# Optimization experiments

Measured on AMD Instinct MI355X. Metric: run time of the kernel, lower is better.

## Reference

```python
import jax, jax.numpy as jnp
import numpy as np

B = 256        # graph pairs
MAX_SET = 64   # nodes per graph == max_set_size (padding is identity)
E = 512        # edges per graph
D = 128        # node_state_dim == av.filters_3
T = 64         # av.transform_dim
N_PROP = 5
N_TIME = 3
TEMP = 0.1
SINK_ITERS = 20
NG = 2 * B
N = NG * MAX_SET
TOT_E = NG * E


def sinkhorn(log_alpha):
    la = log_alpha / TEMP
    for _ in range(SINK_ITERS):
        la = la - jax.nn.logsumexp(la, axis=2, keepdims=True)
        la = la - jax.nn.logsumexp(la, axis=1, keepdims=True)
    return jnp.exp(la)


def setup_inputs() -> dict:
    key = jax.random.key(0)
    ks = jax.random.split(key, 32)

    def lin(k, i, o):
        return jax.random.normal(k, (i, o), jnp.float32) / np.sqrt(i).astype(np.float32)

    node_features = jax.random.normal(ks[0], (N, 32), jnp.float32)
    edge_features = jax.random.normal(ks[1], (TOT_E, 16), jnp.float32)
    offs = jnp.repeat(jnp.arange(NG, dtype=jnp.int32) * MAX_SET, E)
    from_idx = jax.random.randint(ks[2], (TOT_E,), 0, MAX_SET, jnp.int32) + offs
    to_idx = jax.random.randint(ks[3], (TOT_E,), 0, MAX_SET, jnp.int32) + offs
    return {
        "node_features": node_features, "edge_features": edge_features,
        "from_idx": from_idx, "to_idx": to_idx,
        "node_enc_w": lin(ks[4], 32, D), "node_enc_b": jnp.zeros((D,), jnp.float32),
        "edge_enc_w": lin(ks[5], 16, 64), "edge_enc_b": jnp.zeros((64,), jnp.float32),
        "mw1": lin(ks[6], 2 * D + 64, 2 * D), "mb1": jnp.zeros((2 * D,), jnp.float32),
        "mw2": lin(ks[7], 2 * D, D), "mb2": jnp.zeros((D,), jnp.float32),
        "nw1": lin(ks[8], 2 * D, 2 * D), "nb1": jnp.zeros((2 * D,), jnp.float32),
        "nw2": lin(ks[9], 2 * D, D), "nb2": jnp.zeros((D,), jnp.float32),
        "cw1": lin(ks[10], 2 * D, 2 * D), "cb1": jnp.zeros((2 * D,), jnp.float32),
        "cw2": lin(ks[11], 2 * D, D), "cb2": jnp.zeros((D,), jnp.float32),
        "t1w": lin(ks[12], D, T), "t1b": jnp.zeros((T,), jnp.float32),
        "t2w": lin(ks[13], T, T), "t2b": jnp.zeros((T,), jnp.float32),
    }


def reference(node_features, edge_features, from_idx, to_idx,
              node_enc_w, node_enc_b, edge_enc_w, edge_enc_b,
              mw1, mb1, mw2, mb2, nw1, nb1, nw2, nb2,
              cw1, cb1, cw2, cb2, t1w, t1b, t2w, t2b):
    # Encoder (GMN GraphEncoder: linear maps on raw node/edge features)
    h0 = node_features @ node_enc_w + node_enc_b          # [N, D]
    e0 = edge_features @ edge_enc_w + edge_enc_b          # [TOT_E, 64]
    store = jnp.zeros((N, D * (N_PROP + 1)), h0.dtype)    # node_feature_store
    plan = None
    for _t in range(N_TIME):
        h = h0
        parts = [jnp.zeros((N, D), h0.dtype)]             # slot 0 stays zero
        for p in range(1, N_PROP + 1):
            inter = store[:, (p - 1) * D: p * D]          # time_update_idx == 'k_t'
            comb = jax.nn.relu(jnp.concatenate([h, inter], 1) @ cw1 + cb1) @ cw2 + cb2
            # GraphPropLayer: gather -> message MLP -> segment_sum -> node update MLP
            msg_in = jnp.concatenate([comb[from_idx], comb[to_idx], e0], 1)
            messages = jax.nn.relu(msg_in @ mw1 + mb1) @ mw2 + mb2
            agg = jax.ops.segment_sum(messages, to_idx, num_segments=N)
            h = jax.nn.relu(jnp.concatenate([comb, agg], 1) @ nw1 + nb1) @ nw2 + nb2
            parts.append(h)
        store = jnp.concatenate(parts, 1)                 # [N, D*(K+1)]
        # split into padded query/corpus stacks (all graphs have MAX_SET nodes,
        # so F.pad and the size masks are identity here)
        s = store.reshape(NG, MAX_SET, -1)
        q, c = s[0::2], s[1::2]                           # [B, M, D*(K+1)]
        tq = jax.nn.relu(q[:, :, -D:] @ t1w + t1b) @ t2w + t2b
        tc = jax.nn.relu(c[:, :, -D:] @ t1w + t1b) @ t2w + t2b
        sim = jnp.einsum('bqt,bct->bqc', tq, tc)
        plan = sinkhorn(sim)                              # node transport plan [B,M,M]
        qfc = jnp.einsum('bqc,bcd->bqd', plan, c)
        cfq = jnp.einsum('bqc,bqd->bcd', plan, q)
        inter_feats = jnp.stack([qfc, cfq], 1)[:, :, :, D:].reshape(N, N_PROP * D)
        store = store.at[:, D:].set(inter_feats)
    return plan
```

## Files before the change

### kernel.cpp

```cpp
#include <hip/hip_runtime.h>
#include <hip/hip_bf16.h>

#define NNODES   32768
#define NGROUPS  512
#define EPG      512
#define ND       (32768l*128)

typedef __attribute__((ext_vector_type(4))) float f32x4;
typedef __attribute__((ext_vector_type(8))) short bf16x8;

__device__ __forceinline__ short f2bf(float x) {
  unsigned u = __float_as_uint(x);
  unsigned r = (u + 0x7FFF + ((u >> 16) & 1)) >> 16;
  return (short)r;
}
__device__ __forceinline__ float bf2f(short h) {
  return __uint_as_float(((unsigned)(unsigned short)h) << 16);
}
__device__ __forceinline__ void split3(float x, short* ph, short* pm, short* pl, long idx) {
  short h = f2bf(x); float r1 = x - bf2f(h);
  short m = f2bf(r1); float r2 = r1 - bf2f(m);
  ph[idx] = h; pm[idx] = m; pl[idx] = f2bf(r2);
}

__global__ void k_node_enc(const float* __restrict__ nf, const float* __restrict__ w,
                           const float* __restrict__ b, float* __restrict__ h0) {
  int idx = blockIdx.x * 256 + threadIdx.x;
  int row = idx >> 7, col = idx & 127;
  const float* x = nf + row * 32;
  float acc = b[col];
#pragma unroll
  for (int k = 0; k < 32; ++k) acc = fmaf(x[k], w[k * 128 + col], acc);
  h0[idx] = acc;
}

__global__ void k_prep(const float* __restrict__ eew, const float* __restrict__ eeb,
                       const float* __restrict__ mw1, const float* __restrict__ mb1,
                       const float* __restrict__ mb2, const float* __restrict__ nw1,
                       float* __restrict__ Wfold, float* __restrict__ bfold,
                       float* __restrict__ vbias) {
  const int c = threadIdx.x, b = blockIdx.x;
  if (b < 16) {
    float a = 0.f;
    for (int j = 0; j < 64; ++j) a = fmaf(eew[b * 64 + j], mw1[(256 + j) * 256 + c], a);
    Wfold[b * 256 + c] = a;
  } else if (b == 16) {
    float a = mb1[c];
    for (int j = 0; j < 64; ++j) a = fmaf(eeb[j], mw1[(256 + j) * 256 + c], a);
    bfold[c] = a;
  } else {
    float a = 0.f;
    for (int j = 0; j < 128; ++j) a = fmaf(mb2[j], nw1[(128 + j) * 256 + c], a);
    vbias[c] = a;
  }
}

__global__ void k_wsplit3(const float* __restrict__ W, int C, int Kd,
                          short* __restrict__ th, short* __restrict__ tm,
                          short* __restrict__ tl) {
  const int c = blockIdx.x;
  for (int k = threadIdx.x; k < Kd; k += 256) {
    float w = W[(long)k * C + c];
    split3(w, th, tm, tl, c * 256 + k);
  }
}

__global__ void k_csr(const int* __restrict__ from_idx, const int* __restrict__ to_idx,
                      const float* __restrict__ ef,
                      int* __restrict__ csr_f, int* __restrict__ rp_g,
                      float* __restrict__ efp, int* __restrict__ deg) {
  __shared__ int cnt[64], rps[65];
  __shared__ int tls[EPG], fls[EPG];
  __shared__ short ord[EPG];
  const int g = blockIdx.x, tid = threadIdx.x;
  const int be = g * EPG, bn = g * 64;
  if (tid < 64) cnt[tid] = 0;
  __syncthreads();
  for (int e = tid; e < EPG; e += 256) {
    int t = to_idx[be + e] - bn;
    tls[e] = t;
    fls[e] = from_idx[be + e] - bn;
    atomicAdd(&cnt[t], 1);
  }
  __syncthreads();
  if (tid == 0) {
    int s = 0;
    for (int i = 0; i < 64; ++i) { rps[i] = s; s += cnt[i]; }
    rps[64] = s;
  }
  __syncthreads();
  if (tid < 64) {
    int pos = rps[tid];
    for (int e = 0; e < EPG; ++e)
      if (tls[e] == tid) ord[pos++] = (short)e;
  }
  __syncthreads();
  for (int ec = tid; ec < EPG; ec += 256) {
    const int eo = ord[ec];
    csr_f[be + ec] = fls[eo];
    const float4* src = (const float4*)&ef[(long)(be + eo) * 16];
    float4* dst = (float4*)&efp[(long)(be + ec) * 16];
    dst[0] = src[0]; dst[1] = src[1]; dst[2] = src[2]; dst[3] = src[3];
  }
  if (tid < 65) rp_g[g * 65 + tid] = rps[tid];
  if (tid < 64) deg[bn + tid] = cnt[tid];
}

template<int KTOT, bool DEG, bool SUM2, bool RPX0, bool WPOUT>
__global__ __launch_bounds__(256, 3)
void k_mlp2m(const float* __restrict__ x0,
             const short* __restrict__ x0h, const short* __restrict__ x0m,
             const short* __restrict__ x0l,
             const float* __restrict__ x1, const float* __restrict__ x1b,
             const short* __restrict__ W1h, const short* __restrict__ W1m,
             const short* __restrict__ W1l,
             const float* __restrict__ b1, const int* __restrict__ deg,
             const float* __restrict__ vbias,
             const short* __restrict__ W2h, const short* __restrict__ W2m,
             const short* __restrict__ W2l,
             const float* __restrict__ b2,
             float* __restrict__ out,
             short* __restrict__ outh, short* __restrict__ outm,
             short* __restrict__ outl) {
  __shared__ short xh[32 * 264];
  __shared__ short xm[32 * 264];
  __shared__ short xl[32 * 264];
  __shared__ int degs[32];
  const int tid = threadIdx.x;
  const long row0 = (long)blockIdx.x * 32;

  if constexpr (RPX0) {
    for (int i = tid; i < 32 * 16; i += 256) {
      const int r = i >> 4, q = i & 15;
      const long gb = (row0 + r) * 128 + q * 8;
      const int lb = r * 264 + q * 8;
      *(bf16x8*)&xh[lb] = *(const bf16x8*)&x0h[gb];
      *(bf16x8*)&xm[lb] = *(const bf16x8*)&x0m[gb];
      *(bf16x8*)&xl[lb] = *(const bf16x8*)&x0l[gb];
    }
  } else {
    for (int i = tid; i < 32 * 32; i += 256) {
      const int r = i >> 5, q = i & 31;
      float4 v = *(const float4*)&x0[(row0 + r) * 128 + q * 4];
      const int base = r * 264 + q * 4;
      split3(v.x, xh, xm, xl, base + 0);
      split3(v.y, xh, xm, xl, base + 1);
      split3(v.z, xh, xm, xl, base + 2);
      split3(v.w, xh, xm, xl, base + 3);
    }
  }
  if constexpr (KTOT == 256) {
    for (int i = tid; i < 32 * 32; i += 256) {
      const int r = i >> 5, q = i & 31;
      float4 v = *(const float4*)&x1[(row0 + r) * 128 + q * 4];
      if constexpr (SUM2) {
        float4 w = *(const float4*)&x1b[(row0 + r) * 128 + q * 4];
        v.x += w.x; v.y += w.y; v.z += w.z; v.w += w.w;
      }
      const int base = r * 264 + 128 + q * 4;
      split3(v.x, xh, xm, xl, base + 0);
      split3(v.y, xh, xm, xl, base + 1);
      split3(v.z, xh, xm, xl, base + 2);
      split3(v.w, xh, xm, xl, base + 3);
    }
  }
  if constexpr (DEG) { if (tid < 32) degs[tid] = deg[row0 + tid]; }
  __syncthreads();

  const int lane = tid & 63, wid = tid >> 6;
  const int lr = lane & 15;
  const int lk = (lane >> 4) * 8;
  const int rsub = (lane >> 4) * 4;

  f32x4 acc[2][4];
#pragma unroll
  for (int fc = 0; fc < 4; ++fc) {
    const int col = wid * 64 + fc * 16 + lr;
    const float bv = b1[col];
#pragma unroll
    for (int fr = 0; fr < 2; ++fr) acc[fr][fc] = {bv, bv, bv, bv};
    if constexpr (DEG) {
      const float vb = vbias[col];
#pragma unroll
      for (int fr = 0; fr < 2; ++fr)
#pragma unroll
        for (int r = 0; r < 4; ++r)
          acc[fr][fc][r] += (float)degs[fr * 16 + rsub + r] * vb;
    }
  }

#pragma unroll 2
  for (int ks = 0; ks < KTOT / 32; ++ks) {
    const int k0 = ks * 32 + lk;
    bf16x8 ah[2], am[2], al[2];
#pragma unroll
    for (int fr = 0; fr < 2; ++fr) {
      const int ab = (fr * 16 + lr) * 264 + k0;
      ah[fr] = *(const bf16x8*)&xh[ab];
      am[fr] = *(const bf16x8*)&xm[ab];
      al[fr] = *(const bf16x8*)&xl[ab];
    }
#pragma unroll
    for (int fc = 0; fc < 4; ++fc) {
      const long wrow = (long)(wid * 64 + fc * 16 + lr) * 256 + k0;
      const bf16x8 bh = *(const bf16x8*)&W1h[wrow];
      const bf16x8 bm = *(const bf16x8*)&W1m[wrow];
      const bf16x8 bl = *(const bf16x8*)&W1l[wrow];
#pragma unroll
      for (int fr = 0; fr < 2; ++fr) {
        acc[fr][fc] = __builtin_amdgcn_mfma_f32_16x16x32_bf16(ah[fr], bh, acc[fr][fc], 0, 0, 0);
        acc[fr][fc] = __builtin_amdgcn_mfma_f32_16x16x32_bf16(ah[fr], bm, acc[fr][fc], 0, 0, 0);
        acc[fr][fc] = __builtin_amdgcn_mfma_f32_16x16x32_bf16(am[fr], bh, acc[fr][fc], 0, 0, 0);
        acc[fr][fc] = __builtin_amdgcn_mfma_f32_16x16x32_bf16(ah[fr], bl, acc[fr][fc], 0, 0, 0);
        acc[fr][fc] = __builtin_amdgcn_mfma_f32_16x16x32_bf16(am[fr], bm, acc[fr][fc], 0, 0, 0);
        acc[fr][fc] = __builtin_amdgcn_mfma_f32_16x16x32_bf16(al[fr], bh, acc[fr][fc], 0, 0, 0);
      }
    }
  }
  __syncthreads();

#pragma unroll
  for (int fr = 0; fr < 2; ++fr)
#pragma unroll
    for (int fc = 0; fc < 4; ++fc) {
      const int col = wid * 64 + fc * 16 + lr;
#pragma unroll
      for (int r = 0; r < 4; ++r) {
        const int row = fr * 16 + rsub + r;
        float v = fmaxf(acc[fr][fc][r], 0.f);
        split3(v, xh, xm, xl, row * 264 + col);
      }
    }
  __syncthreads();

  f32x4 acc2[2][2];
#pragma unroll
  for (int fc = 0; fc < 2; ++fc) {
    const float bv = b2[wid * 32 + fc * 16 + lr];
#pragma unroll
    for (int fr = 0; fr < 2; ++fr) acc2[fr][fc] = {bv, bv, bv, bv};
  }
#pragma unroll 2
  for (int ks = 0; ks < 8; ++ks) {
    const int k0 = ks * 32 + lk;
    bf16x8 ah[2], am[2], al[2];
#pragma unroll
    for (int fr = 0; fr < 2; ++fr) {
      const int ab = (fr * 16 + lr) * 264 + k0;
      ah[fr] = *(const bf16x8*)&xh[ab];
      am[fr] = *(const bf16x8*)&xm[ab];
      al[fr] = *(const bf16x8*)&xl[ab];
    }
#pragma unroll
    for (int fc = 0; fc < 2; ++fc) {
      const long wrow = (long)(wid * 32 + fc * 16 + lr) * 256 + k0;
      const bf16x8 bh = *(const bf16x8*)&W2h[wrow];
      const bf16x8 bm = *(const bf16x8*)&W2m[wrow];
      const bf16x8 bl = *(const bf16x8*)&W2l[wrow];
#pragma unroll
      for (int fr = 0; fr < 2; ++fr) {
        acc2[fr][fc] = __builtin_amdgcn_mfma_f32_16x16x32_bf16(ah[fr], bh, acc2[fr][fc], 0, 0, 0);
        acc2[fr][fc] = __builtin_amdgcn_mfma_f32_16x16x32_bf16(ah[fr], bm, acc2[fr][fc], 0, 0, 0);
        acc2[fr][fc] = __builtin_amdgcn_mfma_f32_16x16x32_bf16(am[fr], bh, acc2[fr][fc], 0, 0, 0);
        acc2[fr][fc] = __builtin_amdgcn_mfma_f32_16x16x32_bf16(ah[fr], bl, acc2[fr][fc], 0, 0, 0);
        acc2[fr][fc] = __builtin_amdgcn_mfma_f32_16x16x32_bf16(am[fr], bm, acc2[fr][fc], 0, 0, 0);
        acc2[fr][fc] = __builtin_amdgcn_mfma_f32_16x16x32_bf16(al[fr], bh, acc2[fr][fc], 0, 0, 0);
      }
    }
  }
#pragma unroll
  for (int fr = 0; fr < 2; ++fr)
#pragma unroll
    for (int fc = 0; fc < 2; ++fc) {
      const int col = wid * 32 + fc * 16 + lr;
#pragma unroll
      for (int r = 0; r < 4; ++r) {
        const long gi = (row0 + fr * 16 + rsub + r) * 128 + col;
        if constexpr (WPOUT) {
          split3(acc2[fr][fc][r], outh, outm, outl, gi);
        } else {
          out[gi] = acc2[fr][fc][r];
        }
      }
    }
}

__global__ __launch_bounds__(256, 3)
void k_edgem(const short* __restrict__ chp, const short* __restrict__ cmp,
             const short* __restrict__ clp,
             const float* __restrict__ efp,
             const short* __restrict__ m1h, const short* __restrict__ m1m,
             const short* __restrict__ m1l,
             const short* __restrict__ m2h, const short* __restrict__ m2m,
             const short* __restrict__ m2l,
             const float* __restrict__ Wfold, const float* __restrict__ bfold,
             const int* __restrict__ csr_f, const int* __restrict__ rp_g,
             float* __restrict__ aggM) {
  __shared__ __align__(16) float cAB[2 * 64 * 68];
  __shared__ __align__(16) float ag[64 * 64];
  __shared__ short fl[EPG];
  __shared__ int rp[65];
  float* cA = cAB;
  float* cB = cAB + 64 * 68;
  short* agp = (short*)cAB;

  const int tid = threadIdx.x;
  const int g = blockIdx.x, half = blockIdx.y;
  const int be = g * EPG, bn = g * 64;

  for (int i = tid; i < EPG; i += 256) fl[i] = (short)csr_f[be + i];
  if (tid < 65) rp[tid] = rp_g[g * 65 + tid];

  const int lane = tid & 63, wid = tid >> 6;
  const int lr = lane & 15;
  const int lk = (lane >> 4) * 8;
  const int rsub = (lane >> 4) * 4;
  const int ng = tid >> 4, cg = tid & 15;
  const int n0 = ng * 4, cq = cg * 4;

  float* aggMh = aggM + (long)half * ND;

  for (int cbi = 0; cbi < 2; ++cbi) {
    const int col0 = (half * 2 + cbi) * 64;
    __syncthreads();

    {
      const int isB = wid >> 1;
      const int cw = (wid & 1) * 32;
      const int wkof = isB * 128;
      float* dstC = isB ? cB : cA;
#pragma unroll 1
      for (int hf = 0; hf < 2; ++hf) {
        f32x4 c[2][2];
#pragma unroll
        for (int fr = 0; fr < 2; ++fr)
#pragma unroll
          for (int fc = 0; fc < 2; ++fc) c[fr][fc] = {0.f, 0.f, 0.f, 0.f};
        for (int ks = 0; ks < 4; ++ks) {
          const int k0 = ks * 32 + lk;
          bf16x8 ah[2], am[2], al[2];
#pragma unroll
          for (int fr = 0; fr < 2; ++fr) {
            const long ga = (long)(bn + (hf * 2 + fr) * 16 + lr) * 128 + k0;
            ah[fr] = *(const bf16x8*)&chp[ga];
            am[fr] = *(const bf16x8*)&cmp[ga];
            al[fr] = *(const bf16x8*)&clp[ga];
          }
#pragma unroll
          for (int fc = 0; fc < 2; ++fc) {
            const long wrow = (long)(col0 + cw + fc * 16 + lr) * 256 + wkof + k0;
            const bf16x8 bh = *(const bf16x8*)&m1h[wrow];
            const bf16x8 bm = *(const bf16x8*)&m1m[wrow];
            const bf16x8 bl = *(const bf16x8*)&m1l[wrow];
#pragma unroll
            for (int fr = 0; fr < 2; ++fr) {
              c[fr][fc] = __builtin_amdgcn_mfma_f32_16x16x32_bf16(ah[fr], bh, c[fr][fc], 0, 0, 0);
              c[fr][fc] = __builtin_amdgcn_mfma_f32_16x16x32_bf16(ah[fr], bm, c[fr][fc], 0, 0, 0);
              c[fr][fc] = __builtin_amdgcn_mfma_f32_16x16x32_bf16(am[fr], bh, c[fr][fc], 0, 0, 0);
              c[fr][fc] = __builtin_amdgcn_mfma_f32_16x16x32_bf16(ah[fr], bl, c[fr][fc], 0, 0, 0);
              c[fr][fc] = __builtin_amdgcn_mfma_f32_16x16x32_bf16(am[fr], bm, c[fr][fc], 0, 0, 0);
              c[fr][fc] = __builtin_amdgcn_mfma_f32_16x16x32_bf16(al[fr], bh, c[fr][fc], 0, 0, 0);
            }
          }
        }
#pragma unroll
        for (int fr = 0; fr < 2; ++fr)
#pragma unroll
          for (int fc = 0; fc < 2; ++fc) {
            const int col = cw + fc * 16 + lr;
#pragma unroll
            for (int r = 0; r < 4; ++r)
              dstC[((hf * 2 + fr) * 16 + rsub + r) * 68 + col] = c[fr][fc][r];
          }
      }
    }
    float4 Wf[16];
#pragma unroll
    for (int k = 0; k < 16; ++k) Wf[k] = *(const float4*)&Wfold[k * 256 + col0 + cq];
    const float4 bf = *(const float4*)&bfold[col0 + cq];
    __syncthreads();

#pragma unroll
    for (int i = 0; i < 4; ++i) {
      const int n = n0 + i;
      const float4 cBn = *(const float4*)&cB[n * 68 + cq];
      const int eBeg = rp[n], eEnd = rp[n + 1];
      float4 acc0 = make_float4(0.f, 0.f, 0.f, 0.f);
      float4 acc1 = make_float4(0.f, 0.f, 0.f, 0.f);
      int e = eBeg;
      for (; e + 1 < eEnd; e += 2) {
        const int f0 = fl[e], f1 = fl[e + 1];
        const float* er0 = efp + (long)(be + e) * 16;
        const float* er1 = efp + (long)(be + e + 1) * 16;
        float4 ea[4], eb[4];
#pragma unroll
        for (int kq = 0; kq < 4; ++kq) { ea[kq] = ((const float4*)er0)[kq]; eb[kq] = ((const float4*)er1)[kq]; }
        float4 h0 = bf, h1 = bf;
#pragma unroll
        for (int kq = 0; kq < 4; ++kq) {
          const float ev0[4] = {ea[kq].x, ea[kq].y, ea[kq].z, ea[kq].w};
          const float ev1[4] = {eb[kq].x, eb[kq].y, eb[kq].z, eb[kq].w};
#pragma unroll
          for (int s = 0; s < 4; ++s) {
            const float4 w = Wf[kq * 4 + s];
            h0.x = fmaf(ev0[s], w.x, h0.x); h0.y = fmaf(ev0[s], w.y, h0.y);
            h0.z = fmaf(ev0[s], w.z, h0.z); h0.w = fmaf(ev0[s], w.w, h0.w);
            h1.x = fmaf(ev1[s], w.x, h1.x); h1.y = fmaf(ev1[s], w.y, h1.y);
            h1.z = fmaf(ev1[s], w.z, h1.z); h1.w = fmaf(ev1[s], w.w, h1.w);
          }
        }
        const float4 va0 = *(const float4*)&cA[f0 * 68 + cq];
        const float4 va1 = *(const float4*)&cA[f1 * 68 + cq];
        acc0.x += fmaxf(h0.x + va0.x + cBn.x, 0.f);
        acc0.y += fmaxf(h0.y + va0.y + cBn.y, 0.f);
        acc0.z += fmaxf(h0.z + va0.z + cBn.z, 0.f);
        acc0.w += fmaxf(h0.w + va0.w + cBn.w, 0.f);
        acc1.x += fmaxf(h1.x + va1.x + cBn.x, 0.f);
        acc1.y += fmaxf(h1.y + va1.y + cBn.y, 0.f);
        acc1.z += fmaxf(h1.z + va1.z + cBn.z, 0.f);
        acc1.w += fmaxf(h1.w + va1.w + cBn.w, 0.f);
      }
      if (e < eEnd) {
        const int f = fl[e];
        const float* er = efp + (long)(be + e) * 16;
        float4 h = bf;
#pragma unroll
        for (int kq = 0; kq < 4; ++kq) {
          const float4 e4 = ((const float4*)er)[kq];
          const float ev[4] = {e4.x, e4.y, e4.z, e4.w};
#pragma unroll
          for (int s = 0; s < 4; ++s) {
            const float4 w = Wf[kq * 4 + s];
            h.x = fmaf(ev[s], w.x, h.x); h.y = fmaf(ev[s], w.y, h.y);
            h.z = fmaf(ev[s], w.z, h.z); h.w = fmaf(ev[s], w.w, h.w);
          }
        }
        const float4 va = *(const float4*)&cA[f * 68 + cq];
        acc0.x += fmaxf(h.x + va.x + cBn.x, 0.f);
        acc0.y += fmaxf(h.y + va.y + cBn.y, 0.f);
        acc0.z += fmaxf(h.z + va.z + cBn.z, 0.f);
        acc0.w += fmaxf(h.w + va.w + cBn.w, 0.f);
      }
      acc0.x += acc1.x; acc0.y += acc1.y; acc0.z += acc1.z; acc0.w += acc1.w;
      *(float4*)&ag[n * 64 + cq] = acc0;
    }
    __syncthreads();

    for (int i = tid; i < 1024; i += 256) {
      const int n = i >> 4, kq = (i & 15) * 4;
      const float4 v = *(const float4*)&ag[n * 64 + kq];
      const int b0 = n * 72 + kq;
      split3(v.x, agp, agp + 4608, agp + 9216, b0 + 0);
      split3(v.y, agp, agp + 4608, agp + 9216, b0 + 1);
      split3(v.z, agp, agp + 4608, agp + 9216, b0 + 2);
      split3(v.w, agp, agp + 4608, agp + 9216, b0 + 3);
    }
    __syncthreads();

    {
      f32x4 aM2[4][2];
#pragma unroll
      for (int fr = 0; fr < 4; ++fr)
#pragma unroll
        for (int fc = 0; fc < 2; ++fc) aM2[fr][fc] = {0.f, 0.f, 0.f, 0.f};

      for (int ks = 0; ks < 2; ++ks) {
        const int k0 = ks * 32 + lk;
        bf16x8 ah[4], am[4], al[4];
#pragma unroll
        for (int fr = 0; fr < 4; ++fr) {
          const int ab = (fr * 16 + lr) * 72 + k0;
          ah[fr] = *(const bf16x8*)&agp[ab];
          am[fr] = *(const bf16x8*)&agp[4608 + ab];
          al[fr] = *(const bf16x8*)&agp[9216 + ab];
        }
#pragma unroll
        for (int fc = 0; fc < 2; ++fc) {
          const long wrow = (long)(wid * 32 + fc * 16 + lr) * 256 + col0 + k0;
          const bf16x8 bh = *(const bf16x8*)&m2h[wrow];
          const bf16x8 bm = *(const bf16x8*)&m2m[wrow];
          const bf16x8 bl = *(const bf16x8*)&m2l[wrow];
#pragma unroll
          for (int fr = 0; fr < 4; ++fr) {
            aM2[fr][fc] = __builtin_amdgcn_mfma_f32_16x16x32_bf16(ah[fr], bh, aM2[fr][fc], 0, 0, 0);
            aM2[fr][fc] = __builtin_amdgcn_mfma_f32_16x16x32_bf16(ah[fr], bm, aM2[fr][fc], 0, 0, 0);
            aM2[fr][fc] = __builtin_amdgcn_mfma_f32_16x16x32_bf16(am[fr], bh, aM2[fr][fc], 0, 0, 0);
            aM2[fr][fc] = __builtin_amdgcn_mfma_f32_16x16x32_bf16(ah[fr], bl, aM2[fr][fc], 0, 0, 0);
            aM2[fr][fc] = __builtin_amdgcn_mfma_f32_16x16x32_bf16(am[fr], bm, aM2[fr][fc], 0, 0, 0);
            aM2[fr][fc] = __builtin_amdgcn_mfma_f32_16x16x32_bf16(al[fr], bh, aM2[fr][fc], 0, 0, 0);
          }
        }
      }
      if (cbi == 0) {
#pragma unroll
        for (int fr = 0; fr < 4; ++fr)
#pragma unroll
          for (int fc = 0; fc < 2; ++fc) {
            const int col = wid * 32 + fc * 16 + lr;
#pragma unroll
            for (int r = 0; r < 4; ++r)
              aggMh[(long)(bn + fr * 16 + rsub + r) * 128 + col] = aM2[fr][fc][r];
          }
      } else {
#pragma unroll
        for (int fr = 0; fr < 4; ++fr)
#pragma unroll
          for (int fc = 0; fc < 2; ++fc) {
            const int col = wid * 32 + fc * 16 + lr;
#pragma unroll
            for (int r = 0; r < 4; ++r)
              atomicAdd(&aggMh[(long)(bn + fr * 16 + rsub + r) * 128 + col], aM2[fr][fc][r]);
          }
      }
    }
  }
}

__global__ void k_tfeat(const float* __restrict__ x,
                        const float* __restrict__ t1w, const float* __restrict__ t1b,
                        const float* __restrict__ t2w, const float* __restrict__ t2b,
                        float* __restrict__ tf) {
  __shared__ float xs[4][128];
  __shared__ float ys[4][64];
  const int tid = threadIdx.x;
  const long row0 = (long)blockIdx.x * 4;
  for (int i = tid; i < 512; i += 256)
    xs[i >> 7][i & 127] = x[(row0 + (i >> 7)) * 128 + (i & 127)];
  __syncthreads();
  const int r = tid >> 6, c = tid & 63;
  float acc = t1b[c];
#pragma unroll 4
  for (int k = 0; k < 128; ++k) acc = fmaf(xs[r][k], t1w[k * 64 + c], acc);
  ys[r][c] = fmaxf(acc, 0.f);
  __syncthreads();
  float a2 = t2b[c];
#pragma unroll 4
  for (int k = 0; k < 64; ++k) a2 = fmaf(ys[r][k], t2w[k * 64 + c], a2);
  tf[(row0 + r) * 64 + c] = a2;
}

__global__ void k_sim(const float* __restrict__ tf, float* __restrict__ sim) {
  const int b = blockIdx.x, tid = threadIdx.x;
  __shared__ float tq[64][65];
  __shared__ float tcs[64][65];
  for (int i = tid; i < 4096; i += 256) {
    tq[i >> 6][i & 63]  = tf[(long)b * 8192 + i];
    tcs[i >> 6][i & 63] = tf[(long)b * 8192 + 4096 + i];
  }
  __syncthreads();
  const int m = tid >> 2, j0 = (tid & 3) * 16;
#pragma unroll
  for (int j = 0; j < 16; ++j) {
    float a = 0.f;
#pragma unroll 4
    for (int k = 0; k < 64; ++k) a = fmaf(tq[m][k], tcs[j0 + j][k], a);
    sim[(long)b * 4096 + m * 64 + j0 + j] = a;
  }
}

__global__ void k_sink(float* __restrict__ sim, float* __restrict__ outp) {
  const int b = blockIdx.x, tid = threadIdx.x;
  __shared__ float la[64][65];
  const float C = 14.426950408889634f;
  for (int i = tid; i < 4096; i += 256)
    la[i >> 6][i & 63] = sim[(long)b * 4096 + i] * C;
  __syncthreads();
  const int r4 = tid >> 2, l4 = tid & 3;
  for (int it = 0; it < 20; ++it) {
    {
      float m = -3.4e38f;
#pragma unroll
      for (int i = 0; i < 16; ++i) m = fmaxf(m, la[r4][l4 + 4 * i]);
      m = fmaxf(m, __shfl_xor(m, 1)); m = fmaxf(m, __shfl_xor(m, 2));
      float s = 0.f;
#pragma unroll
      for (int i = 0; i < 16; ++i) s += exp2f(la[r4][l4 + 4 * i] - m);
      s += __shfl_xor(s, 1); s += __shfl_xor(s, 2);
      const float lse = m + log2f(s);
#pragma unroll
      for (int i = 0; i < 16; ++i) la[r4][l4 + 4 * i] -= lse;
    }
    __syncthreads();
    {
      float m = -3.4e38f;
#pragma unroll
      for (int i = 0; i < 16; ++i) m = fmaxf(m, la[l4 + 4 * i][r4]);
      m = fmaxf(m, __shfl_xor(m, 1)); m = fmaxf(m, __shfl_xor(m, 2));
      float s = 0.f;
#pragma unroll
      for (int i = 0; i < 16; ++i) s += exp2f(la[l4 + 4 * i][r4] - m);
      s += __shfl_xor(s, 1); s += __shfl_xor(s, 2);
      const float lse = m + log2f(s);
#pragma unroll
      for (int i = 0; i < 16; ++i) la[l4 + 4 * i][r4] -= lse;
    }
    __syncthreads();
  }
  for (int i = tid; i < 4096; i += 256) {
    const float v = exp2f(la[i >> 6][i & 63]);
    outp[(long)b * 4096 + i] = v;
    sim[(long)b * 4096 + i] = v;
  }
}

__global__ void k_mix(const float* __restrict__ plan, const float* __restrict__ src,
                      float* __restrict__ dst) {
  const int b = blockIdx.x, tid = threadIdx.x;
  __shared__ float pl[64][65];
  __shared__ float qs[64][128];
  __shared__ float cs[64][128];
  const long qbase = (long)(2 * b) * 64, cbase = qbase + 64;
  for (int i = tid; i < 4096; i += 256) pl[i >> 6][i & 63] = plan[(long)b * 4096 + i];
  for (int i = tid; i < 8192; i += 256) {
    qs[i >> 7][i & 127] = src[qbase * 128 + i];
    cs[i >> 7][i & 127] = src[cbase * 128 + i];
  }
  __syncthreads();
  const int d = tid & 127, m0 = (tid >> 7) * 32;
  for (int m = m0; m < m0 + 32; ++m) {
    float a = 0.f;
#pragma unroll 4
    for (int j = 0; j < 64; ++j) a = fmaf(pl[m][j], cs[j][d], a);
    dst[(qbase + m) * 128 + d] = a;
  }
  for (int j = m0; j < m0 + 32; ++j) {
    float a = 0.f;
#pragma unroll 4
    for (int m = 0; m < 64; ++m) a = fmaf(pl[m][j], qs[m][d], a);
    dst[(cbase + j) * 128 + d] = a;
  }
}

extern "C" void kernel_launch(void* const* d_in, const int* in_sizes, int n_in,
                              void* d_out, int out_size, void* d_ws, size_t ws_size,
                              hipStream_t stream) {
  const float* nf  = (const float*)d_in[0];
  const float* ef  = (const float*)d_in[1];
  const int* from_idx = (const int*)d_in[2];
  const int* to_idx   = (const int*)d_in[3];
  const float* new_w = (const float*)d_in[4];
  const float* new_b = (const float*)d_in[5];
  const float* eew = (const float*)d_in[6];
  const float* eeb = (const float*)d_in[7];
  const float* mw1 = (const float*)d_in[8];
  const float* mb1 = (const float*)d_in[9];
  const float* mw2 = (const float*)d_in[10];
  const float* mb2 = (const float*)d_in[11];
  const float* nw1 = (const float*)d_in[12];
  const float* nb1 = (const float*)d_in[13];
  const float* nw2 = (const float*)d_in[14];
  const float* nb2 = (const float*)d_in[15];
  const float* cw1 = (const float*)d_in[16];
  const float* cb1 = (const float*)d_in[17];
  const float* cw2 = (const float*)d_in[18];
  const float* cb2 = (const float*)d_in[19];
  const float* t1w = (const float*)d_in[20];
  const float* t1b = (const float*)d_in[21];
  const float* t2w = (const float*)d_in[22];
  const float* t2b = (const float*)d_in[23];

  float* W = (float*)d_ws;
  float* h0     = W;
  float* aggM0  = h0 + ND;
  float* aggM1  = aggM0 + ND;
  float* parts  = aggM1 + ND;
  float* efp    = parts + 5 * ND;
  float* Wfold  = efp + 262144l * 16;
  float* bfold  = Wfold + 4096;
  float* vbias  = bfold + 256;
  int*   deg    = (int*)(vbias + 256);
  int*   csr_f  = deg + 32768;
  int*   rp_g   = csr_f + 262144;
  short* cw1t_h = (short*)(rp_g + 33280);
  short* cw1t_m = cw1t_h + 65536;
  short* cw1t_l = cw1t_m + 65536;
  short* nw1t_h = cw1t_l + 65536;
  short* nw1t_m = nw1t_h + 65536;
  short* nw1t_l = nw1t_m + 65536;
  short* cw2t_h = nw1t_l + 65536;
  short* cw2t_m = cw2t_h + 32768;
  short* cw2t_l = cw2t_m + 32768;
  short* nw2t_h = cw2t_l + 32768;
  short* nw2t_m = nw2t_h + 32768;
  short* nw2t_l = nw2t_m + 32768;
  short* m1t_h  = nw2t_l + 32768;
  short* m1t_m  = m1t_h + 65536;
  short* m1t_l  = m1t_m + 65536;
  short* m2t_h  = m1t_l + 65536;
  short* m2t_m  = m2t_h + 32768;
  short* m2t_l  = m2t_m + 32768;
  short* chp    = m2t_l + 32768;
  short* cmp    = chp + 32768l * 128;
  short* clp    = cmp + 32768l * 128;
  float* tf     = aggM0;
  float* sim    = aggM0 + 2097152;
  float* outp   = (float*)d_out;

  k_prep<<<18, 256, 0, stream>>>(eew, eeb, mw1, mb1, mb2, nw1, Wfold, bfold, vbias);
  k_csr<<<512, 256, 0, stream>>>(from_idx, to_idx, ef, csr_f, rp_g, efp, deg);
  k_wsplit3<<<256, 256, 0, stream>>>(cw1, 256, 256, cw1t_h, cw1t_m, cw1t_l);
  k_wsplit3<<<256, 256, 0, stream>>>(nw1, 256, 256, nw1t_h, nw1t_m, nw1t_l);
  k_wsplit3<<<128, 256, 0, stream>>>(cw2, 128, 256, cw2t_h, cw2t_m, cw2t_l);
  k_wsplit3<<<128, 256, 0, stream>>>(nw2, 128, 256, nw2t_h, nw2t_m, nw2t_l);
  k_wsplit3<<<256, 256, 0, stream>>>(mw1, 256, 256, m1t_h, m1t_m, m1t_l);
  k_wsplit3<<<128, 256, 0, stream>>>(mw2, 128, 256, m2t_h, m2t_m, m2t_l);
  k_node_enc<<<16384, 256, 0, stream>>>(nf, new_w, new_b, h0);

  for (int t = 0; t < 3; ++t) {
    const float* hprev = h0;
    for (int p = 1; p <= 5; ++p) {
      if (t > 0 && p > 1)
        k_mlp2m<256, false, false, false, true><<<1024, 256, 0, stream>>>(
            hprev, nullptr, nullptr, nullptr,
            parts + (long)(p - 1) * ND, nullptr,
            cw1t_h, cw1t_m, cw1t_l, cb1, nullptr, nullptr,
            cw2t_h, cw2t_m, cw2t_l, cb2, nullptr, chp, cmp, clp);
      else
        k_mlp2m<128, false, false, false, true><<<1024, 256, 0, stream>>>(
            hprev, nullptr, nullptr, nullptr, nullptr, nullptr,
            cw1t_h, cw1t_m, cw1t_l, cb1, nullptr, nullptr,
            cw2t_h, cw2t_m, cw2t_l, cb2, nullptr, chp, cmp, clp);
      k_edgem<<<dim3(512, 2), 256, 0, stream>>>(chp, cmp, clp, efp,
                                                m1t_h, m1t_m, m1t_l,
                                                m2t_h, m2t_m, m2t_l,
                                                Wfold, bfold, csr_f, rp_g, aggM0);
      float* hnew = parts + (long)(p - 1) * ND;
      k_mlp2m<256, true, true, true, false><<<1024, 256, 0, stream>>>(
          nullptr, chp, cmp, clp, aggM0, aggM1,
          nw1t_h, nw1t_m, nw1t_l, nb1, deg, vbias,
          nw2t_h, nw2t_m, nw2t_l, nb2, hnew, nullptr, nullptr, nullptr);
      hprev = hnew;
    }
    k_tfeat<<<8192, 256, 0, stream>>>(parts + 4 * ND, t1w, t1b, t2w, t2b, tf);
    k_sim<<<256, 256, 0, stream>>>(tf, sim);
    k_sink<<<256, 256, 0, stream>>>(sim, outp);
    if (t < 2) {
      for (int pi = 3; pi >= 0; --pi)
        k_mix<<<256, 256, 0, stream>>>(sim, parts + (long)pi * ND, parts + (long)(pi + 1) * ND);
    }
  }
}
```

Baseline: 6.118 ms.

## Split edge kernel into hidden-aggregation and separate mw2 GEMM kernels

The fused edge kernel used to compute the 256-wide hidden aggregate in two column halves, each applying mw2 and combining partial results through atomics and a second buffer. It is now split in two. An edge kernel over 4 column blocks writes the full aggregated hidden tensor to global memory, and a separate dense GEMM kernel applies mw2 with K=256, so the atomics and the SUM2 addition in the node MLP go away. This adds a global round trip of a 2*ND float buffer and one extra launch per propagation step, in exchange for more parallelism and simpler GEMM tiling.

```diff
diff --git a/kernel.cpp b/kernel.cpp
--- a/kernel.cpp
+++ b/kernel.cpp
@@ -106,12 +106,12 @@
   if (tid < 64) deg[bn + tid] = cnt[tid];
 }
 
-template<int KTOT, bool DEG, bool SUM2, bool RPX0, bool WPOUT>
+template<int KTOT, bool DEG, bool RPX0, bool WPOUT>
 __global__ __launch_bounds__(256, 3)
 void k_mlp2m(const float* __restrict__ x0,
              const short* __restrict__ x0h, const short* __restrict__ x0m,
              const short* __restrict__ x0l,
-             const float* __restrict__ x1, const float* __restrict__ x1b,
+             const float* __restrict__ x1,
              const short* __restrict__ W1h, const short* __restrict__ W1m,
              const short* __restrict__ W1l,
              const float* __restrict__ b1, const int* __restrict__ deg,
@@ -153,10 +153,6 @@
     for (int i = tid; i < 32 * 32; i += 256) {
       const int r = i >> 5, q = i & 31;
       float4 v = *(const float4*)&x1[(row0 + r) * 128 + q * 4];
-      if constexpr (SUM2) {
-        float4 w = *(const float4*)&x1b[(row0 + r) * 128 + q * 4];
-        v.x += w.x; v.y += w.y; v.z += w.z; v.w += w.w;
-      }
       const int base = r * 264 + 128 + q * 4;
       split3(v.x, xh, xm, xl, base + 0);
       split3(v.y, xh, xm, xl, base + 1);
@@ -286,27 +282,24 @@
 }
 
 __global__ __launch_bounds__(256, 3)
-void k_edgem(const short* __restrict__ chp, const short* __restrict__ cmp,
+void k_edgeb(const short* __restrict__ chp, const short* __restrict__ cmp,
              const short* __restrict__ clp,
              const float* __restrict__ efp,
              const short* __restrict__ m1h, const short* __restrict__ m1m,
              const short* __restrict__ m1l,
-             const short* __restrict__ m2h, const short* __restrict__ m2m,
-             const short* __restrict__ m2l,
              const float* __restrict__ Wfold, const float* __restrict__ bfold,
              const int* __restrict__ csr_f, const int* __restrict__ rp_g,
-             float* __restrict__ aggM) {
+             float* __restrict__ ag) {
   __shared__ __align__(16) float cAB[2 * 64 * 68];
-  __shared__ __align__(16) float ag[64 * 64];
   __shared__ short fl[EPG];
   __shared__ int rp[65];
   float* cA = cAB;
   float* cB = cAB + 64 * 68;
-  short* agp = (short*)cAB;
 
   const int tid = threadIdx.x;
-  const int g = blockIdx.x, half = blockIdx.y;
+  const int g = blockIdx.x, cb = blockIdx.y;
   const int be = g * EPG, bn = g * 64;
+  const int col0 = cb * 64;
 
   for (int i = tid; i < EPG; i += 256) fl[i] = (short)csr_f[be + i];
   if (tid < 65) rp[tid] = rp_g[g * 65 + tid];
@@ -318,202 +311,225 @@
   const int ng = tid >> 4, cg = tid & 15;
   const int n0 = ng * 4, cq = cg * 4;
 
-  float* aggMh = aggM + (long)half * ND;
-
-  for (int cbi = 0; cbi < 2; ++cbi) {
-    const int col0 = (half * 2 + cbi) * 64;
-    __syncthreads();
-
-    {
-      const int isB = wid >> 1;
-      const int cw = (wid & 1) * 32;
-      const int wkof = isB * 128;
-      float* dstC = isB ? cB : cA;
+  {
+    const int isB = wid >> 1;
+    const int cw = (wid & 1) * 32;
+    const int wkof = isB * 128;
+    float* dstC = isB ? cB : cA;
 #pragma unroll 1
-      for (int hf = 0; hf < 2; ++hf) {
-        f32x4 c[2][2];
-#pragma unroll
-        for (int fr = 0; fr < 2; ++fr)
-#pragma unroll
-          for (int fc = 0; fc < 2; ++fc) c[fr][fc] = {0.f, 0.f, 0.f, 0.f};
-        for (int ks = 0; ks < 4; ++ks) {
-          const int k0 = ks * 32 + lk;
-          bf16x8 ah[2], am[2], al[2];
+    for (int hf = 0; hf < 2; ++hf) {
+      f32x4 c[2][2];
+#pragma unroll
+      for (int fr = 0; fr < 2; ++fr)
+#pragma unroll
+        for (int fc = 0; fc < 2; ++fc) c[fr][fc] = {0.f, 0.f, 0.f, 0.f};
+      for (int ks = 0; ks < 4; ++ks) {
+        const int k0 = ks * 32 + lk;
+        bf16x8 ah[2], am[2], al[2];
+#pragma unroll
+        for (int fr = 0; fr < 2; ++fr) {
+          const long ga = (long)(bn + (hf * 2 + fr) * 16 + lr) * 128 + k0;
+          ah[fr] = *(const bf16x8*)&chp[ga];
+          am[fr] = *(const bf16x8*)&cmp[ga];
+          al[fr] = *(const bf16x8*)&clp[ga];
+        }
+#pragma unroll
+        for (int fc = 0; fc < 2; ++fc) {
+          const long wrow = (long)(col0 + cw + fc * 16 + lr) * 256 + wkof + k0;
+          const bf16x8 bh = *(const bf16x8*)&m1h[wrow];
+          const bf16x8 bm = *(const bf16x8*)&m1m[wrow];
+          const bf16x8 bl = *(const bf16x8*)&m1l[wrow];
 #pragma unroll
           for (int fr = 0; fr < 2; ++fr) {
-            const long ga = (long)(bn + (hf * 2 + fr) * 16 + lr) * 128 + k0;
-            ah[fr] = *(const bf16x8*)&chp[ga];
-            am[fr] = *(const bf16x8*)&cmp[ga];
-            al[fr] = *(const bf16x8*)&clp[ga];
-          }
-#pragma unroll
-          for (int fc = 0; fc < 2; ++fc) {
-            const long wrow = (long)(col0 + cw + fc * 16 + lr) * 256 + wkof + k0;
-            const bf16x8 bh = *(const bf16x8*)&m1h[wrow];
-            const bf16x8 bm = *(const bf16x8*)&m1m[wrow];
-            const bf16x8 bl = *(const bf16x8*)&m1l[wrow];
-#pragma unroll
-            for (int fr = 0; fr < 2; ++fr) {
-              c[fr][fc] = __builtin_amdgcn_mfma_f32_16x16x32_bf16(ah[fr], bh, c[fr][fc], 0, 0, 0);
-              c[fr][fc] = __builtin_amdgcn_mfma_f32_16x16x32_bf16(ah[fr], bm, c[fr][fc], 0, 0, 0);
-              c[fr][fc] = __builtin_amdgcn_mfma_f32_16x16x32_bf16(am[fr], bh, c[fr][fc], 0, 0, 0);
-              c[fr][fc] = __builtin_amdgcn_mfma_f32_16x16x32_bf16(ah[fr], bl, c[fr][fc], 0, 0, 0);
-              c[fr][fc] = __builtin_amdgcn_mfma_f32_16x16x32_bf16(am[fr], bm, c[fr][fc], 0, 0, 0);
-              c[fr][fc] = __builtin_amdgcn_mfma_f32_16x16x32_bf16(al[fr], bh, c[fr][fc], 0, 0, 0);
-            }
+            c[fr][fc] = __builtin_amdgcn_mfma_f32_16x16x32_bf16(ah[fr], bh, c[fr][fc], 0, 0, 0);
+            c[fr][fc] = __builtin_amdgcn_mfma_f32_16x16x32_bf16(ah[fr], bm, c[fr][fc], 0, 0, 0);
+            c[fr][fc] = __builtin_amdgcn_mfma_f32_16x16x32_bf16(am[fr], bh, c[fr][fc], 0, 0, 0);
+            c[fr][fc] = __builtin_amdgcn_mfma_f32_16x16x32_bf16(ah[fr], bl, c[fr][fc], 0, 0, 0);
+            c[fr][fc] = __builtin_amdgcn_mfma_f32_16x16x32_bf16(am[fr], bm, c[fr][fc], 0, 0, 0);
+            c[fr][fc] = __builtin_amdgcn_mfma_f32_16x16x32_bf16(al[fr], bh, c[fr][fc], 0, 0, 0);
           }
         }
-#pragma unroll
-        for (int fr = 0; fr < 2; ++fr)
-#pragma unroll
-          for (int fc = 0; fc < 2; ++fc) {
-            const int col = cw + fc * 16 + lr;
-#pragma unroll
-            for (int r = 0; r < 4; ++r)
-              dstC[((hf * 2 + fr) * 16 + rsub + r) * 68 + col] = c[fr][fc][r];
-          }
-      }
-    }
-    float4 Wf[16];
-#pragma unroll
-    for (int k = 0; k < 16; ++k) Wf[k] = *(const float4*)&Wfold[k * 256 + col0 + cq];
-    const float4 bf = *(const float4*)&bfold[col0 + cq];
-    __syncthreads();
-
-#pragma unroll
-    for (int i = 0; i < 4; ++i) {
-      const int n = n0 + i;
-      const float4 cBn = *(const float4*)&cB[n * 68 + cq];
-      const int eBeg = rp[n], eEnd = rp[n + 1];
-      float4 acc0 = make_float4(0.f, 0.f, 0.f, 0.f);
-      float4 acc1 = make_float4(0.f, 0.f, 0.f, 0.f);
-      int e = eBeg;
-      for (; e + 1 < eEnd; e += 2) {
-        const int f0 = fl[e], f1 = fl[e + 1];
-        const float* er0 = efp + (long)(be + e) * 16;
-        const float* er1 = efp + (long)(be + e + 1) * 16;
-        float4 ea[4], eb[4];
-#pragma unroll
-        for (int kq = 0; kq < 4; ++kq) { ea[kq] = ((const float4*)er0)[kq]; eb[kq] = ((const float4*)er1)[kq]; }
-        float4 h0 = bf, h1 = bf;
-#pragma unroll
-        for (int kq = 0; kq < 4; ++kq) {
-          const float ev0[4] = {ea[kq].x, ea[kq].y, ea[kq].z, ea[kq].w};
-          const float ev1[4] = {eb[kq].x, eb[kq].y, eb[kq].z, eb[kq].w};
-#pragma unroll
-          for (int s = 0; s < 4; ++s) {
-            const float4 w = Wf[kq * 4 + s];
-            h0.x = fmaf(ev0[s], w.x, h0.x); h0.y = fmaf(ev0[s], w.y, h0.y);
-            h0.z = fmaf(ev0[s], w.z, h0.z); h0.w = fmaf(ev0[s], w.w, h0.w);
-            h1.x = fmaf(ev1[s], w.x, h1.x); h1.y = fmaf(ev1[s], w.y, h1.y);
-            h1.z = fmaf(ev1[s], w.z, h1.z); h1.w = fmaf(ev1[s], w.w, h1.w);
-          }
+      }
+#pragma unroll
+      for (int fr = 0; fr < 2; ++fr)
+#pragma unroll
+        for (int fc = 0; fc < 2; ++fc) {
+          const int col = cw + fc * 16 + lr;
+#pragma unroll
+          for (int r = 0; r < 4; ++r)
+            dstC[((hf * 2 + fr) * 16 + rsub + r) * 68 + col] = c[fr][fc][r];
         }
-        const float4 va0 = *(const float4*)&cA[f0 * 68 + cq];
-        const float4 va1 = *(const float4*)&cA[f1 * 68 + cq];
-        acc0.x += fmaxf(h0.x + va0.x + cBn.x, 0.f);
-        acc0.y += fmaxf(h0.y + va0.y + cBn.y, 0.f);
-        acc0.z += fmaxf(h0.z + va0.z + cBn.z, 0.f);
-        acc0.w += fmaxf(h0.w + va0.w + cBn.w, 0.f);
-        acc1.x += fmaxf(h1.x + va1.x + cBn.x, 0.f);
-        acc1.y += fmaxf(h1.y + va1.y + cBn.y, 0.f);
-        acc1.z += fmaxf(h1.z + va1.z + cBn.z, 0.f);
-        acc1.w += fmaxf(h1.w + va1.w + cBn.w, 0.f);
-      }
-      if (e < eEnd) {
-        const int f = fl[e];
-        const float* er = efp + (long)(be + e) * 16;
-        float4 h = bf;
-#pragma unroll
-        for (int kq = 0; kq < 4; ++kq) {
-          const float4 e4 = ((const float4*)er)[kq];
-          const float ev[4] = {e4.x, e4.y, e4.z, e4.w};
-#pragma unroll
-          for (int s = 0; s < 4; ++s) {
-            const float4 w = Wf[kq * 4 + s];
-            h.x = fmaf(ev[s], w.x, h.x); h.y = fmaf(ev[s], w.y, h.y);
-            h.z = fmaf(ev[s], w.z, h.z); h.w = fmaf(ev[s], w.w, h.w);
-          }
+    }
+  }
+  float4 Wf[16];
+#pragma unroll
+  for (int k = 0; k < 16; ++k) Wf[k] = *(const float4*)&Wfold[k * 256 + col0 + cq];
+  const float4 bf = *(const float4*)&bfold[col0 + cq];
+  __syncthreads();
+
+#pragma unroll
+  for (int i = 0; i < 4; ++i) {
+    const int n = n0 + i;
+    const float4 cBn = *(const float4*)&cB[n * 68 + cq];
+    const int eBeg = rp[n], eEnd = rp[n + 1];
+    float4 acc0 = make_float4(0.f, 0.f, 0.f, 0.f);
+    float4 acc1 = make_float4(0.f, 0.f, 0.f, 0.f);
+    int e = eBeg;
+    for (; e + 1 < eEnd; e += 2) {
+      const int f0 = fl[e], f1 = fl[e + 1];
+      const float* er0 = efp + (long)(be + e) * 16;
+      const float* er1 = efp + (long)(be + e + 1) * 16;
+      float4 ea[4], eb[4];
+#pragma unroll
+      for (int kq = 0; kq < 4; ++kq) { ea[kq] = ((const float4*)er0)[kq]; eb[kq] = ((const float4*)er1)[kq]; }
+      float4 h0 = bf, h1 = bf;
+#pragma unroll
+      for (int kq = 0; kq < 4; ++kq) {
+        const float ev0[4] = {ea[kq].x, ea[kq].y, ea[kq].z, ea[kq].w};
+        const float ev1[4] = {eb[kq].x, eb[kq].y, eb[kq].z, eb[kq].w};
+#pragma unroll
+        for (int s = 0; s < 4; ++s) {
+          const float4 w = Wf[kq * 4 + s];
+          h0.x = fmaf(ev0[s], w.x, h0.x); h0.y = fmaf(ev0[s], w.y, h0.y);
+          h0.z = fmaf(ev0[s], w.z, h0.z); h0.w = fmaf(ev0[s], w.w, h0.w);
+          h1.x = fmaf(ev1[s], w.x, h1.x); h1.y = fmaf(ev1[s], w.y, h1.y);
+          h1.z = fmaf(ev1[s], w.z, h1.z); h1.w = fmaf(ev1[s], w.w, h1.w);
         }
-        const float4 va = *(const float4*)&cA[f * 68 + cq];
-        acc0.x += fmaxf(h.x + va.x + cBn.x, 0.f);
-        acc0.y += fmaxf(h.y + va.y + cBn.y, 0.f);
-        acc0.z += fmaxf(h.z + va.z + cBn.z, 0.f);
-        acc0.w += fmaxf(h.w + va.w + cBn.w, 0.f);
-      }
-      acc0.x += acc1.x; acc0.y += acc1.y; acc0.z += acc1.z; acc0.w += acc1.w;
-      *(float4*)&ag[n * 64 + cq] = acc0;
-    }
-    __syncthreads();
-
-    for (int i = tid; i < 1024; i += 256) {
-      const int n = i >> 4, kq = (i & 15) * 4;
-      const float4 v = *(const float4*)&ag[n * 64 + kq];
-      const int b0 = n * 72 + kq;
-      split3(v.x, agp, agp + 4608, agp + 9216, b0 + 0);
-      split3(v.y, agp, agp + 4608, agp + 9216, b0 + 1);
-      split3(v.z, agp, agp + 4608, agp + 9216, b0 + 2);
-      split3(v.w, agp, agp + 4608, agp + 9216, b0 + 3);
-    }
-    __syncthreads();
-
-    {
-      f32x4 aM2[4][2];
-#pragma unroll
-      for (int fr = 0; fr < 4; ++fr)
-#pragma unroll
-        for (int fc = 0; fc < 2; ++fc) aM2[fr][fc] = {0.f, 0.f, 0.f, 0.f};
-
-      for (int ks = 0; ks < 2; ++ks) {
-        const int k0 = ks * 32 + lk;
-        bf16x8 ah[4], am[4], al[4];
-#pragma unroll
-        for (int fr = 0; fr < 4; ++fr) {
-          const int ab = (fr * 16 + lr) * 72 + k0;
-          ah[fr] = *(const bf16x8*)&agp[ab];
-          am[fr] = *(const bf16x8*)&agp[4608 + ab];
-          al[fr] = *(const bf16x8*)&agp[9216 + ab];
+      }
+      const float4 va0 = *(const float4*)&cA[f0 * 68 + cq];
+      const float4 va1 = *(const float4*)&cA[f1 * 68 + cq];
+      acc0.x += fmaxf(h0.x + va0.x + cBn.x, 0.f);
+      acc0.y += fmaxf(h0.y + va0.y + cBn.y, 0.f);
+      acc0.z += fmaxf(h0.z + va0.z + cBn.z, 0.f);
+      acc0.w += fmaxf(h0.w + va0.w + cBn.w, 0.f);
+      acc1.x += fmaxf(h1.x + va1.x + cBn.x, 0.f);
+      acc1.y += fmaxf(h1.y + va1.y + cBn.y, 0.f);
+      acc1.z += fmaxf(h1.z + va1.z + cBn.z, 0.f);
+      acc1.w += fmaxf(h1.w + va1.w + cBn.w, 0.f);
+    }
+    if (e < eEnd) {
+      const int f = fl[e];
+      const float* er = efp + (long)(be + e) * 16;
+      float4 h = bf;
+#pragma unroll
+      for (int kq = 0; kq < 4; ++kq) {
+        const float4 e4 = ((const float4*)er)[kq];
+        const float ev[4] = {e4.x, e4.y, e4.z, e4.w};
+#pragma unroll
+        for (int s = 0; s < 4; ++s) {
+          const float4 w = Wf[kq * 4 + s];
+          h.x = fmaf(ev[s], w.x, h.x); h.y = fmaf(ev[s], w.y, h.y);
+          h.z = fmaf(ev[s], w.z, h.z); h.w = fmaf(ev[s], w.w, h.w);
         }
-#pragma unroll
-        for (int fc = 0; fc < 2; ++fc) {
-          const long wrow = (long)(wid * 32 + fc * 16 + lr) * 256 + col0 + k0;
-          const bf16x8 bh = *(const bf16x8*)&m2h[wrow];
-          const bf16x8 bm = *(const bf16x8*)&m2m[wrow];
-          const bf16x8 bl = *(const bf16x8*)&m2l[wrow];
-#pragma unroll
-          for (int fr = 0; fr < 4; ++fr) {
-            aM2[fr][fc] = __builtin_amdgcn_mfma_f32_16x16x32_bf16(ah[fr], bh, aM2[fr][fc], 0, 0, 0);
-            aM2[fr][fc] = __builtin_amdgcn_mfma_f32_16x16x32_bf16(ah[fr], bm, aM2[fr][fc], 0, 0, 0);
-            aM2[fr][fc] = __builtin_amdgcn_mfma_f32_16x16x32_bf16(am[fr], bh, aM2[fr][fc], 0, 0, 0);
-            aM2[fr][fc] = __builtin_amdgcn_mfma_f32_16x16x32_bf16(ah[fr], bl, aM2[fr][fc], 0, 0, 0);
-            aM2[fr][fc] = __builtin_amdgcn_mfma_f32_16x16x32_bf16(am[fr], bm, aM2[fr][fc], 0, 0, 0);
-            aM2[fr][fc] = __builtin_amdgcn_mfma_f32_16x16x32_bf16(al[fr], bh, aM2[fr][fc], 0, 0, 0);
-          }
-        }
-      }
-      if (cbi == 0) {
-#pragma unroll
-        for (int fr = 0; fr < 4; ++fr)
-#pragma unroll
-          for (int fc = 0; fc < 2; ++fc) {
-            const int col = wid * 32 + fc * 16 + lr;
-#pragma unroll
-            for (int r = 0; r < 4; ++r)
-              aggMh[(long)(bn + fr * 16 + rsub + r) * 128 + col] = aM2[fr][fc][r];
-          }
-      } else {
-#pragma unroll
-        for (int fr = 0; fr < 4; ++fr)
-#pragma unroll
-          for (int fc = 0; fc < 2; ++fc) {
-            const int col = wid * 32 + fc * 16 + lr;
-#pragma unroll
-            for (int r = 0; r < 4; ++r)
-              atomicAdd(&aggMh[(long)(bn + fr * 16 + rsub + r) * 128 + col], aM2[fr][fc][r]);
-          }
-      }
-    }
-  }
+      }
+      const float4 va = *(const float4*)&cA[f * 68 + cq];
+      acc0.x += fmaxf(h.x + va.x + cBn.x, 0.f);
+      acc0.y += fmaxf(h.y + va.y + cBn.y, 0.f);
+      acc0.z += fmaxf(h.z + va.z + cBn.z, 0.f);
+      acc0.w += fmaxf(h.w + va.w + cBn.w, 0.f);
+    }
+    acc0.x += acc1.x; acc0.y += acc1.y; acc0.z += acc1.z; acc0.w += acc1.w;
+    *(float4*)&ag[(long)(bn + n) * 256 + col0 + cq] = acc0;
+  }
+}
+
+__global__ __launch_bounds__(256, 3)
+void k_aggm(const float* __restrict__ ag,
+            const short* __restrict__ m2h, const short* __restrict__ m2m,
+            const short* __restrict__ m2l, float* __restrict__ aggM) {
+  __shared__ short xh[32 * 264];
+  __shared__ short xm[32 * 264];
+  __shared__ short xl[32 * 264];
+  const int tid = threadIdx.x;
+  const long row0 = (long)blockIdx.x * 32;
+
+  for (int i = tid; i < 2048; i += 256) {
+    const int r = i >> 6, q = i & 63;
+    float4 v = *(const float4*)&ag[(row0 + r) * 256 + q * 4];
+    const int base = r * 264 + q * 4;
+    split3(v.x, xh, xm, xl, base + 0);
+    split3(v.y, xh, xm, xl, base + 1);
+    split3(v.z, xh, xm, xl, base + 2);
+    split3(v.w, xh, xm, xl, base + 3);
+  }
+  __syncthreads();
+
+  const int lane = tid & 63, wid = tid >> 6;
+  const int lr = lane & 15;
+  const int lk = (lane >> 4) * 8;
+  const int rsub = (lane >> 4) * 4;
+
+  f32x4 s0[2][2], s1[2][2];
+#pragma unroll
+  for (int fc = 0; fc < 2; ++fc)
+#pragma unroll
+    for (int fr = 0; fr < 2; ++fr) { s0[fr][fc] = {0.f, 0.f, 0.f, 0.f}; s1[fr][fc] = {0.f, 0.f, 0.f, 0.f}; }
+
+#pragma unroll 2
+  for (int ks = 0; ks < 4; ++ks) {
+    const int k0 = ks * 32 + lk;
+    bf16x8 ah[2], am[2], al[2];
+#pragma unroll
+    for (int fr = 0; fr < 2; ++fr) {
+      const int ab = (fr * 16 + lr) * 264 + k0;
+      ah[fr] = *(const bf16x8*)&xh[ab];
+      am[fr] = *(const bf16x8*)&xm[ab];
+      al[fr] = *(const bf16x8*)&xl[ab];
+    }
+#pragma unroll
+    for (int fc = 0; fc < 2; ++fc) {
+      const long wrow = (long)(wid * 32 + fc * 16 + lr) * 256 + k0;
+      const bf16x8 bh = *(const bf16x8*)&m2h[wrow];
+      const bf16x8 bm = *(const bf16x8*)&m2m[wrow];
+      const bf16x8 bl = *(const bf16x8*)&m2l[wrow];
+#pragma unroll
+      for (int fr = 0; fr < 2; ++fr) {
+        s0[fr][fc] = __builtin_amdgcn_mfma_f32_16x16x32_bf16(ah[fr], bh, s0[fr][fc], 0, 0, 0);
+        s0[fr][fc] = __builtin_amdgcn_mfma_f32_16x16x32_bf16(ah[fr], bm, s0[fr][fc], 0, 0, 0);
+        s0[fr][fc] = __builtin_amdgcn_mfma_f32_16x16x32_bf16(am[fr], bh, s0[fr][fc], 0, 0, 0);
+        s0[fr][fc] = __builtin_amdgcn_mfma_f32_16x16x32_bf16(ah[fr], bl, s0[fr][fc], 0, 0, 0);
+        s0[fr][fc] = __builtin_amdgcn_mfma_f32_16x16x32_bf16(am[fr], bm, s0[fr][fc], 0, 0, 0);
+        s0[fr][fc] = __builtin_amdgcn_mfma_f32_16x16x32_bf16(al[fr], bh, s0[fr][fc], 0, 0, 0);
+      }
+    }
+  }
+#pragma unroll 2
+  for (int ks = 4; ks < 8; ++ks) {
+    const int k0 = ks * 32 + lk;
+    bf16x8 ah[2], am[2], al[2];
+#pragma unroll
+    for (int fr = 0; fr < 2; ++fr) {
+      const int ab = (fr * 16 + lr) * 264 + k0;
+      ah[fr] = *(const bf16x8*)&xh[ab];
+      am[fr] = *(const bf16x8*)&xm[ab];
+      al[fr] = *(const bf16x8*)&xl[ab];
+    }
+#pragma unroll
+    for (int fc = 0; fc < 2; ++fc) {
+      const long wrow = (long)(wid * 32 + fc * 16 + lr) * 256 + k0;
+      const bf16x8 bh = *(const bf16x8*)&m2h[wrow];
+      const bf16x8 bm = *(const bf16x8*)&m2m[wrow];
+      const bf16x8 bl = *(const bf16x8*)&m2l[wrow];
+#pragma unroll
+      for (int fr = 0; fr < 2; ++fr) {
+        s1[fr][fc] = __builtin_amdgcn_mfma_f32_16x16x32_bf16(ah[fr], bh, s1[fr][fc], 0, 0, 0);
+        s1[fr][fc] = __builtin_amdgcn_mfma_f32_16x16x32_bf16(ah[fr], bm, s1[fr][fc], 0, 0, 0);
+        s1[fr][fc] = __builtin_amdgcn_mfma_f32_16x16x32_bf16(am[fr], bh, s1[fr][fc], 0, 0, 0);
+        s1[fr][fc] = __builtin_amdgcn_mfma_f32_16x16x32_bf16(ah[fr], bl, s1[fr][fc], 0, 0, 0);
+        s1[fr][fc] = __builtin_amdgcn_mfma_f32_16x16x32_bf16(am[fr], bm, s1[fr][fc], 0, 0, 0);
+        s1[fr][fc] = __builtin_amdgcn_mfma_f32_16x16x32_bf16(al[fr], bh, s1[fr][fc], 0, 0, 0);
+      }
+    }
+  }
+#pragma unroll
+  for (int fr = 0; fr < 2; ++fr)
+#pragma unroll
+    for (int fc = 0; fc < 2; ++fc) {
+      const int col = wid * 32 + fc * 16 + lr;
+#pragma unroll
+      for (int r = 0; r < 4; ++r)
+        aggM[(row0 + fr * 16 + rsub + r) * 128 + col] = s0[fr][fc][r] + s1[fr][fc][r];
+    }
 }
 
 __global__ void k_tfeat(const float* __restrict__ x,
@@ -662,8 +678,8 @@
   float* W = (float*)d_ws;
   float* h0     = W;
   float* aggM0  = h0 + ND;
-  float* aggM1  = aggM0 + ND;
-  float* parts  = aggM1 + ND;
+  float* ag     = aggM0 + ND;
+  float* parts  = ag + 2 * ND;
   float* efp    = parts + 5 * ND;
   float* Wfold  = efp + 262144l * 16;
   float* bfold  = Wfold + 4096;
@@ -710,23 +726,23 @@
     const float* hprev = h0;
     for (int p = 1; p <= 5; ++p) {
       if (t > 0 && p > 1)
-        k_mlp2m<256, false, false, false, true><<<1024, 256, 0, stream>>>(
+        k_mlp2m<256, false, false, true><<<1024, 256, 0, stream>>>(
             hprev, nullptr, nullptr, nullptr,
-            parts + (long)(p - 1) * ND, nullptr,
+            parts + (long)(p - 1) * ND,
             cw1t_h, cw1t_m, cw1t_l, cb1, nullptr, nullptr,
             cw2t_h, cw2t_m, cw2t_l, cb2, nullptr, chp, cmp, clp);
       else
-        k_mlp2m<128, false, false, false, true><<<1024, 256, 0, stream>>>(
-            hprev, nullptr, nullptr, nullptr, nullptr, nullptr,
+        k_mlp2m<128, false, false, true><<<1024, 256, 0, stream>>>(
+            hprev, nullptr, nullptr, nullptr, nullptr,
             cw1t_h, cw1t_m, cw1t_l, cb1, nullptr, nullptr,
             cw2t_h, cw2t_m, cw2t_l, cb2, nullptr, chp, cmp, clp);
-      k_edgem<<<dim3(512, 2), 256, 0, stream>>>(chp, cmp, clp, efp,
+      k_edgeb<<<dim3(512, 4), 256, 0, stream>>>(chp, cmp, clp, efp,
                                                 m1t_h, m1t_m, m1t_l,
-                                                m2t_h, m2t_m, m2t_l,
-                                                Wfold, bfold, csr_f, rp_g, aggM0);
+                                                Wfold, bfold, csr_f, rp_g, ag);
+      k_aggm<<<1024, 256, 0, stream>>>(ag, m2t_h, m2t_m, m2t_l, aggM0);
       float* hnew = parts + (long)(p - 1) * ND;
-      k_mlp2m<256, true, true, true, false><<<1024, 256, 0, stream>>>(
-          nullptr, chp, cmp, clp, aggM0, aggM1,
+      k_mlp2m<256, true, true, false><<<1024, 256, 0, stream>>>(
+          nullptr, chp, cmp, clp, aggM0,
           nw1t_h, nw1t_m, nw1t_l, nb1, deg, vbias,
           nw2t_h, nw2t_m, nw2t_l, nb2, hnew, nullptr, nullptr, nullptr);
       hprev = hnew;
```

New measurement: 5.611 ms. 8.3% less time.
